# Optimization experiments

Measured on AMD Instinct MI355X. Metric: run time of the kernel, lower is better.

The kernel has to match this reference:

```python
import jax, jax.numpy as jnp
import numpy as np

C = 256          # num_channel
CE = C // 4      # encoded channels = 64
T = 16           # seq_len
K = 7            # filter_size
D = 1            # dilation
G = 4            # num_groups
PAD = ((K - 1) * D) // 2  # 3
K2G = K * K * G  # 196
EPS = 1e-5


def _bn(x, gamma, beta, mean, var):
    # inference-mode BatchNorm3d over channel axis 1
    inv = gamma * jax.lax.rsqrt(var + EPS)
    return x * inv[None, :, None, None, None] + (beta - mean * inv)[None, :, None, None, None]


def _conv1x1(x, w):
    # x: (B, Cin, T, H, W), w: (Cout, Cin) -> (B, Cout, T, H, W)
    return jnp.einsum('bcthw,oc->bothw', x, w)


def _correlation(x, filter_weight):
    # x: (B, CE, T, H, W); filter_weight: (CE, T, K, K)
    B, c, t, h, w = x.shape
    # x1: temporal shift (repeat first frame)
    x1 = jnp.concatenate([x[:, :, :1], x[:, :, :-1]], axis=2)
    x2 = jnp.pad(x, ((0, 0), (0, 0), (0, 0), (PAD, PAD), (PAD, PAD)))
    outs = []
    for ky in range(K):          # dy outer (torch meshgrid 'ij' order)
        for kx in range(K):
            dy, dx = ky * D, kx * D
            wgt = filter_weight[:, :, ky, kx]  # (CE, T)
            r = wgt[None, :, :, None, None] * x1 * x2[:, :, :, dy:dy + h, dx:dx + w]
            r = r.reshape(B, G, c // G, t, h, w).mean(axis=2)  # (B, G, T, H, W)
            outs.append(r)
    return jnp.concatenate(outs, axis=1)  # (B, K^2*G, T, H, W)


def setup_inputs() -> dict:
    key = jax.random.key(0)
    ks = jax.random.split(key, 12)
    B, H, W = 4, 56, 56
    inp = {
        'x': jax.random.normal(ks[0], (B, C, T, H, W), jnp.float32),
        'enc_w': jax.random.normal(ks[1], (CE, C), jnp.float32) * (2.0 / C) ** 0.5,
        'enc_gamma': jax.random.uniform(ks[2], (CE,), jnp.float32, 0.5, 1.5),
        'enc_beta': jax.random.normal(ks[3], (CE,), jnp.float32) * 0.1,
        'enc_mean': jax.random.normal(ks[4], (CE,), jnp.float32) * 0.1,
        'enc_var': jax.random.uniform(ks[5], (CE,), jnp.float32, 0.5, 1.5),
        'filter_weight': jax.random.normal(ks[6], (CE, T, K, K), jnp.float32) * (2.0 / (T * K * K)) ** 0.5,
        'dec_w': jax.random.normal(ks[7], (C, K2G), jnp.float32) * (2.0 / K2G) ** 0.5,
        'dec_gamma': jax.random.uniform(ks[8], (C,), jnp.float32, 0.5, 1.5),
        'dec_beta': jax.random.normal(ks[9], (C,), jnp.float32) * 0.1,
        'dec_mean': jax.random.normal(ks[10], (C,), jnp.float32) * 0.1,
        'dec_var': jax.random.uniform(ks[11], (C,), jnp.float32, 0.5, 1.5),
    }
    return inp


def reference(x, enc_w, enc_gamma, enc_beta, enc_mean, enc_var,
              filter_weight, dec_w, dec_gamma, dec_beta, dec_mean, dec_var):
    x_enc = jax.nn.relu(_bn(_conv1x1(x, enc_w), enc_gamma, enc_beta, enc_mean, enc_var))
    x_corr = _correlation(x_enc, filter_weight)
    x_dec = _bn(_conv1x1(x_corr, dec_w), dec_gamma, dec_beta, dec_mean, dec_var)
    return jax.nn.relu(x + x_dec)
```

## Files before the change

kernel.cpp:

```cpp
#include <hip/hip_runtime.h>

#define CC   256
#define CEE  64
#define TT   16
#define KKK  7
#define PADK 3
#define GGG  4
#define CGP  16
#define K2G  196
#define KPAD 224
#define HHH  56
#define WWW  56
#define HW   3136
#define THW  50176
#define BBB  4

typedef _Float16 f16x8 __attribute__((ext_vector_type(8)));
typedef float    f32x4 __attribute__((ext_vector_type(4)));

#define N_XENC   (BBB*CEE*THW)
#define OFF_XENC 0
#define OFF_EWT  (N_XENC)
#define OFF_ESC  (OFF_EWT + CC*CEE)
#define OFF_ESH  (OFF_ESC + CEE)
#define OFF_DWTH (OFF_ESH + CEE)
#define OFF_DSC  (OFF_DWTH + (CC*KPAD)/2)
#define OFF_DSH  (OFF_DSC + CC)

__global__ void prep_kernel(const float* __restrict__ enc_w,
                            const float* __restrict__ eg, const float* __restrict__ eb,
                            const float* __restrict__ em, const float* __restrict__ ev,
                            const float* __restrict__ dec_w,
                            const float* __restrict__ dg, const float* __restrict__ db,
                            const float* __restrict__ dm, const float* __restrict__ dv,
                            float* __restrict__ ewt, float* __restrict__ esc, float* __restrict__ esh,
                            _Float16* __restrict__ dwth, float* __restrict__ dsc, float* __restrict__ dsh) {
    int i = blockIdx.x * blockDim.x + threadIdx.x;
    int n = blockDim.x * gridDim.x;
    for (int idx = i; idx < CC * CEE; idx += n) {
        int c = idx >> 6, o = idx & 63;
        ewt[idx] = enc_w[o * CC + c];
    }
    for (int idx = i; idx < CC * KPAD; idx += n) {
        int o = idx / KPAD;
        int k = idx - o * KPAD;
        int ky = k >> 5, rem = k & 31, gg = rem >> 3, kx = rem & 7;
        float v = 0.f;
        if (kx < 7) v = dec_w[o * K2G + (ky * 7 + kx) * GGG + gg];
        dwth[idx] = (_Float16)v;
    }
    for (int idx = i; idx < CEE; idx += n) {
        float inv = eg[idx] * rsqrtf(ev[idx] + 1e-5f);
        esc[idx] = inv;
        esh[idx] = eb[idx] - em[idx] * inv;
    }
    for (int idx = i; idx < CC; idx += n) {
        float inv = dg[idx] * rsqrtf(dv[idx] + 1e-5f);
        dsc[idx] = inv;
        dsh[idx] = db[idx] - dm[idx] * inv;
    }
}

__global__ void __launch_bounds__(256) enc_kernel(
        const float* __restrict__ x, const float* __restrict__ ewt,
        const float* __restrict__ esc, const float* __restrict__ esh,
        float* __restrict__ xenc) {
    __shared__ float wlds[64 * 64];
    const int tid  = threadIdx.x;
    const int og   = tid >> 6;
    const int lane = tid & 63;
    const int b    = blockIdx.x / 196;
    const int q0   = (blockIdx.x % 196) * 256 + lane * 4;
    const float* xb = x + (size_t)b * CC * THW + q0;

    f32x4 acc[16];
    #pragma unroll
    for (int i = 0; i < 16; ++i) acc[i] = (f32x4){0.f, 0.f, 0.f, 0.f};

    #pragma unroll 1
    for (int chunk = 0; chunk < 4; ++chunk) {
        __syncthreads();
        const float4* src = (const float4*)(ewt + chunk * 4096);
        float4* dst = (float4*)wlds;
        #pragma unroll
        for (int k = 0; k < 4; ++k) dst[k * 256 + tid] = src[k * 256 + tid];
        __syncthreads();

        f32x4 xv[4];
        #pragma unroll
        for (int u = 0; u < 4; ++u)
            xv[u] = *(const f32x4*)(xb + (size_t)(chunk * 64 + u) * THW);

        #pragma unroll 1
        for (int cb = 0; cb < 16; ++cb) {
            f32x4 xvn[4];
            if (cb < 15) {
                #pragma unroll
                for (int u = 0; u < 4; ++u)
                    xvn[u] = *(const f32x4*)(xb + (size_t)(chunk * 64 + (cb + 1) * 4 + u) * THW);
            }
            #pragma unroll
            for (int u = 0; u < 4; ++u) {
                const f32x4* wr = (const f32x4*)(wlds + (cb * 4 + u) * 64 + og * 16);
                #pragma unroll
                for (int oi4 = 0; oi4 < 4; ++oi4) {
                    f32x4 w4 = wr[oi4];
                    acc[oi4 * 4 + 0] += w4[0] * xv[u];
                    acc[oi4 * 4 + 1] += w4[1] * xv[u];
                    acc[oi4 * 4 + 2] += w4[2] * xv[u];
                    acc[oi4 * 4 + 3] += w4[3] * xv[u];
                }
            }
            if (cb < 15) {
                #pragma unroll
                for (int u = 0; u < 4; ++u) xv[u] = xvn[u];
            }
        }
    }

    const size_t outbase = (size_t)b * CEE * THW + q0;
    #pragma unroll
    for (int oi = 0; oi < 16; ++oi) {
        const int o = og * 16 + oi;
        const float sc = esc[o];
        const float sh = esh[o];
        f32x4 v = acc[oi] * sc + sh;
        #pragma unroll
        for (int r = 0; r < 4; ++r) v[r] = v[r] > 0.f ? v[r] : 0.f;
        *(f32x4*)(xenc + outbase + (size_t)o * THW) = v;
    }
}

__global__ void __launch_bounds__(256, 3) corr_dec_kernel(
        const float* __restrict__ x, const float* __restrict__ xenc,
        const float* __restrict__ fw, const _Float16* __restrict__ dwth,
        const float* __restrict__ dsc, const float* __restrict__ dsh,
        float* __restrict__ out) {
    __shared__ _Float16 x2t[64 * 14 * 16];
    __shared__ float wg[64 * 49];
    __shared__ __align__(16) _Float16 corr_h[64 * 40];

    const int tid = threadIdx.x;
    const int g = tid >> 6;
    const int lane = tid & 63;
    const int ph = lane >> 3;
    const int pw = lane & 7;

    const int bx = blockIdx.x;
    const int tile = bx % 49;
    const int t = (bx / 49) & 15;
    const int b = bx / 784;
    const int th0 = (tile / 7) * 8;
    const int tw0 = (tile % 7) * 8;

    for (int i = tid; i < 64 * 224; i += 256) {
        int c = i / 224;
        int rem = i - c * 224;
        int hy = rem >> 4;
        int hx = rem & 15;
        int h = th0 + hy - PADK;
        int w = tw0 + hx - PADK;
        float v = 0.f;
        if (hx < 14 && (unsigned)h < HHH && (unsigned)w < WWW)
            v = xenc[((b * CEE + c) * TT + t) * HW + h * WWW + w];
        x2t[i] = (_Float16)v;
    }
    for (int i = tid; i < 64 * 49; i += 256) {
        int c = i / 49;
        int o = i - c * 49;
        wg[i] = fw[c * (TT * 49) + t * 49 + o] * (1.f / 16.f);
    }
    const int tprev = t > 0 ? t - 1 : 0;
    const int hwp = (th0 + ph) * WWW + (tw0 + pw);
    float x1r[16];
    #pragma unroll
    for (int j = 0; j < 16; ++j)
        x1r[j] = xenc[((b * CEE + g * CGP + j) * TT + tprev) * HW + hwp];

    f32x4 acc[4][4];
    #pragma unroll
    for (int mi = 0; mi < 4; ++mi)
        #pragma unroll
        for (int ni = 0; ni < 4; ++ni)
            acc[mi][ni] = (f32x4){0.f, 0.f, 0.f, 0.f};

    const int r16 = lane & 15;
    const int quad = lane >> 4;

    __syncthreads();

    #pragma unroll 1
    for (int ky = 0; ky < 7; ++ky) {
        float a[7];
        #pragma unroll
        for (int kx = 0; kx < 7; ++kx) a[kx] = 0.f;
        #pragma unroll
        for (int j = 0; j < 16; ++j) {
            const float x1v = x1r[j];
            const int crow = g * CGP + j;
            const _Float16* x2p = &x2t[(crow * 14 + (ph + ky)) * 16 + pw];
            const float* wrow = &wg[crow * 49 + ky * 7];
            #pragma unroll
            for (int kx = 0; kx < 7; ++kx)
                a[kx] += wrow[kx] * (x1v * (float)x2p[kx]);
        }
        f16x8 pk;
        #pragma unroll
        for (int kx = 0; kx < 7; ++kx) pk[kx] = (_Float16)a[kx];
        pk[7] = (_Float16)0.f;
        *(f16x8*)(corr_h + lane * 40 + g * 8) = pk;

        f16x8 af[4];
        #pragma unroll
        for (int mi = 0; mi < 4; ++mi)
            af[mi] = *(const f16x8*)(dwth + (size_t)(g * 64 + mi * 16 + r16) * KPAD
                                     + ky * 32 + quad * 8);

        __syncthreads();

        f16x8 bf[4];
        #pragma unroll
        for (int ni = 0; ni < 4; ++ni)
            bf[ni] = *(const f16x8*)(corr_h + (ni * 16 + r16) * 40 + quad * 8);
        #pragma unroll
        for (int mi = 0; mi < 4; ++mi)
            #pragma unroll
            for (int ni = 0; ni < 4; ++ni)
                acc[mi][ni] = __builtin_amdgcn_mfma_f32_16x16x32_f16(af[mi], bf[ni],
                                                                     acc[mi][ni], 0, 0, 0);
        __syncthreads();
    }

    #pragma unroll
    for (int mi = 0; mi < 4; ++mi) {
        #pragma unroll
        for (int reg = 0; reg < 4; ++reg) {
            const int o = g * 64 + mi * 16 + quad * 4 + reg;
            const float sc = dsc[o];
            const float sh = dsh[o];
            const int obase = ((b * CC + o) * TT + t) * HW;
            #pragma unroll
            for (int ni = 0; ni < 4; ++ni) {
                const int p = ni * 16 + r16;
                const int idx = obase + (th0 + (p >> 3)) * WWW + tw0 + (p & 7);
                float v = acc[mi][ni][reg] * sc + sh;
                float rr = x[idx] + v;
                out[idx] = rr > 0.f ? rr : 0.f;
            }
        }
    }
}

extern "C" void kernel_launch(void* const* d_in, const int* in_sizes, int n_in,
                              void* d_out, int out_size, void* d_ws, size_t ws_size,
                              hipStream_t stream) {
    const float* x     = (const float*)d_in[0];
    const float* enc_w = (const float*)d_in[1];
    const float* eg    = (const float*)d_in[2];
    const float* eb    = (const float*)d_in[3];
    const float* em    = (const float*)d_in[4];
    const float* ev    = (const float*)d_in[5];
    const float* fw    = (const float*)d_in[6];
    const float* dec_w = (const float*)d_in[7];
    const float* dg    = (const float*)d_in[8];
    const float* db    = (const float*)d_in[9];
    const float* dm    = (const float*)d_in[10];
    const float* dv    = (const float*)d_in[11];
    float* out = (float*)d_out;
    float* ws  = (float*)d_ws;

    prep_kernel<<<104, 256, 0, stream>>>(enc_w, eg, eb, em, ev, dec_w, dg, db, dm, dv,
                                         ws + OFF_EWT, ws + OFF_ESC, ws + OFF_ESH,
                                         (_Float16*)(ws + OFF_DWTH),
                                         ws + OFF_DSC, ws + OFF_DSH);
    enc_kernel<<<784, 256, 0, stream>>>(x, ws + OFF_EWT, ws + OFF_ESC, ws + OFF_ESH,
                                        ws + OFF_XENC);
    corr_dec_kernel<<<3136, 256, 0, stream>>>(x, ws + OFF_XENC, fw,
                                              (const _Float16*)(ws + OFF_DWTH),
                                              ws + OFF_DSC, ws + OFF_DSH,
                                              out);
}
```

Before: 849.3 us.

## Run encoder 1x1 conv on FP16 MFMA and batch corr-kernel staging loads

The encoder conv is rewritten to use 16x16x32 f16 MFMA with fp16 weights laid out in a padded buffer. x is converted to fp16 in registers instead of running the fp32 FMA loop with LDS-staged weights, and the grid doubles to 1568 blocks. In the corr/dec kernel the xenc and filter-weight staging loads are batched into registers before the LDS stores, and the dwth fragment loads move earlier to hide latency. Its launch-bounds occupancy hint is also removed. Reduced input precision in the encoder may add numeric error.

```diff
diff --git a/kernel.cpp b/kernel.cpp
--- a/kernel.cpp
+++ b/kernel.cpp
@@ -9,6 +9,7 @@
 #define CGP  16
 #define K2G  196
 #define KPAD 224
+#define EWP  264
 #define HHH  56
 #define WWW  56
 #define HW   3136
@@ -20,12 +21,12 @@
 
 #define N_XENC   (BBB*CEE*THW)
 #define OFF_XENC 0
-#define OFF_EWT  (N_XENC)
-#define OFF_ESC  (OFF_EWT + CC*CEE)
+#define OFF_ESC  (N_XENC)
 #define OFF_ESH  (OFF_ESC + CEE)
 #define OFF_DWTH (OFF_ESH + CEE)
 #define OFF_DSC  (OFF_DWTH + (CC*KPAD)/2)
 #define OFF_DSH  (OFF_DSC + CC)
+#define OFF_EWH  (OFF_DSH + CC)
 
 __global__ void prep_kernel(const float* __restrict__ enc_w,
                             const float* __restrict__ eg, const float* __restrict__ eb,
@@ -33,13 +34,14 @@
                             const float* __restrict__ dec_w,
                             const float* __restrict__ dg, const float* __restrict__ db,
                             const float* __restrict__ dm, const float* __restrict__ dv,
-                            float* __restrict__ ewt, float* __restrict__ esc, float* __restrict__ esh,
+                            _Float16* __restrict__ ewh, float* __restrict__ esc, float* __restrict__ esh,
                             _Float16* __restrict__ dwth, float* __restrict__ dsc, float* __restrict__ dsh) {
     int i = blockIdx.x * blockDim.x + threadIdx.x;
     int n = blockDim.x * gridDim.x;
-    for (int idx = i; idx < CC * CEE; idx += n) {
-        int c = idx >> 6, o = idx & 63;
-        ewt[idx] = enc_w[o * CC + c];
+    for (int idx = i; idx < CEE * EWP; idx += n) {
+        int o = idx / EWP;
+        int k = idx - o * EWP;
+        ewh[idx] = (k < CC) ? (_Float16)enc_w[o * CC + k] : (_Float16)0.f;
     }
     for (int idx = i; idx < CC * KPAD; idx += n) {
         int o = idx / KPAD;
@@ -61,77 +63,71 @@
     }
 }
 
-__global__ void __launch_bounds__(256) enc_kernel(
-        const float* __restrict__ x, const float* __restrict__ ewt,
+__global__ void __launch_bounds__(256, 3) enc_kernel(
+        const float* __restrict__ x, const _Float16* __restrict__ ewh,
         const float* __restrict__ esc, const float* __restrict__ esh,
         float* __restrict__ xenc) {
-    __shared__ float wlds[64 * 64];
     const int tid  = threadIdx.x;
-    const int og   = tid >> 6;
+    const int w    = tid >> 6;
     const int lane = tid & 63;
-    const int b    = blockIdx.x / 196;
-    const int q0   = (blockIdx.x % 196) * 256 + lane * 4;
-    const float* xb = x + (size_t)b * CC * THW + q0;
-
-    f32x4 acc[16];
-    #pragma unroll
-    for (int i = 0; i < 16; ++i) acc[i] = (f32x4){0.f, 0.f, 0.f, 0.f};
-
-    #pragma unroll 1
-    for (int chunk = 0; chunk < 4; ++chunk) {
-        __syncthreads();
-        const float4* src = (const float4*)(ewt + chunk * 4096);
-        float4* dst = (float4*)wlds;
-        #pragma unroll
-        for (int k = 0; k < 4; ++k) dst[k * 256 + tid] = src[k * 256 + tid];
-        __syncthreads();
-
-        f32x4 xv[4];
-        #pragma unroll
-        for (int u = 0; u < 4; ++u)
-            xv[u] = *(const f32x4*)(xb + (size_t)(chunk * 64 + u) * THW);
-
-        #pragma unroll 1
-        for (int cb = 0; cb < 16; ++cb) {
-            f32x4 xvn[4];
-            if (cb < 15) {
-                #pragma unroll
-                for (int u = 0; u < 4; ++u)
-                    xvn[u] = *(const f32x4*)(xb + (size_t)(chunk * 64 + (cb + 1) * 4 + u) * THW);
+    const int r16  = lane & 15;
+    const int quad = lane >> 4;
+    const int b    = blockIdx.x / 392;
+    const int q0   = (blockIdx.x % 392) * 128 + w * 32;
+    const float* xb = x + (size_t)b * CC * THW;
+
+    f32x4 acc[4][2];
+    #pragma unroll
+    for (int mi = 0; mi < 4; ++mi)
+        #pragma unroll
+        for (int ni = 0; ni < 2; ++ni)
+            acc[mi][ni] = (f32x4){0.f, 0.f, 0.f, 0.f};
+
+    #pragma unroll
+    for (int kc = 0; kc < 8; ++kc) {
+        f16x8 af[4];
+        #pragma unroll
+        for (int mi = 0; mi < 4; ++mi)
+            af[mi] = *(const f16x8*)(ewh + (mi * 16 + r16) * EWP + kc * 32 + quad * 8);
+
+        f16x8 bf[2];
+        #pragma unroll
+        for (int ni = 0; ni < 2; ++ni) {
+            float xv[8];
+            #pragma unroll
+            for (int j = 0; j < 8; ++j)
+                xv[j] = xb[(size_t)(kc * 32 + quad * 8 + j) * THW + q0 + ni * 16 + r16];
+            #pragma unroll
+            for (int j = 0; j < 8; ++j)
+                bf[ni][j] = (_Float16)xv[j];
+        }
+
+        #pragma unroll
+        for (int mi = 0; mi < 4; ++mi)
+            #pragma unroll
+            for (int ni = 0; ni < 2; ++ni)
+                acc[mi][ni] = __builtin_amdgcn_mfma_f32_16x16x32_f16(af[mi], bf[ni],
+                                                                     acc[mi][ni], 0, 0, 0);
+    }
+
+    #pragma unroll
+    for (int mi = 0; mi < 4; ++mi) {
+        #pragma unroll
+        for (int reg = 0; reg < 4; ++reg) {
+            const int o = mi * 16 + quad * 4 + reg;
+            const float sc = esc[o];
+            const float sh = esh[o];
+            #pragma unroll
+            for (int ni = 0; ni < 2; ++ni) {
+                const int q = q0 + ni * 16 + r16;
+                float v = acc[mi][ni][reg] * sc + sh;
+                xenc[(size_t)(b * CEE + o) * THW + q] = v > 0.f ? v : 0.f;
             }
-            #pragma unroll
-            for (int u = 0; u < 4; ++u) {
-                const f32x4* wr = (const f32x4*)(wlds + (cb * 4 + u) * 64 + og * 16);
-                #pragma unroll
-                for (int oi4 = 0; oi4 < 4; ++oi4) {
-                    f32x4 w4 = wr[oi4];
-                    acc[oi4 * 4 + 0] += w4[0] * xv[u];
-                    acc[oi4 * 4 + 1] += w4[1] * xv[u];
-                    acc[oi4 * 4 + 2] += w4[2] * xv[u];
-                    acc[oi4 * 4 + 3] += w4[3] * xv[u];
-                }
-            }
-            if (cb < 15) {
-                #pragma unroll
-                for (int u = 0; u < 4; ++u) xv[u] = xvn[u];
-            }
-        }
-    }
-
-    const size_t outbase = (size_t)b * CEE * THW + q0;
-    #pragma unroll
-    for (int oi = 0; oi < 16; ++oi) {
-        const int o = og * 16 + oi;
-        const float sc = esc[o];
-        const float sh = esh[o];
-        f32x4 v = acc[oi] * sc + sh;
-        #pragma unroll
-        for (int r = 0; r < 4; ++r) v[r] = v[r] > 0.f ? v[r] : 0.f;
-        *(f32x4*)(xenc + outbase + (size_t)o * THW) = v;
+        }
     }
 }
 
-__global__ void __launch_bounds__(256, 3) corr_dec_kernel(
+__global__ void __launch_bounds__(256) corr_dec_kernel(
         const float* __restrict__ x, const float* __restrict__ xenc,
         const float* __restrict__ fw, const _Float16* __restrict__ dwth,
         const float* __restrict__ dsc, const float* __restrict__ dsh,
@@ -153,22 +149,46 @@
     const int th0 = (tile / 7) * 8;
     const int tw0 = (tile % 7) * 8;
 
-    for (int i = tid; i < 64 * 224; i += 256) {
-        int c = i / 224;
-        int rem = i - c * 224;
-        int hy = rem >> 4;
-        int hx = rem & 15;
-        int h = th0 + hy - PADK;
-        int w = tw0 + hx - PADK;
-        float v = 0.f;
-        if (hx < 14 && (unsigned)h < HHH && (unsigned)w < WWW)
-            v = xenc[((b * CEE + c) * TT + t) * HW + h * WWW + w];
-        x2t[i] = (_Float16)v;
-    }
-    for (int i = tid; i < 64 * 49; i += 256) {
-        int c = i / 49;
-        int o = i - c * 49;
-        wg[i] = fw[c * (TT * 49) + t * 49 + o] * (1.f / 16.f);
+    {
+        const int bbase = (b * CEE * TT + t) * HW;
+        #pragma unroll 1
+        for (int k0 = 0; k0 < 56; k0 += 8) {
+            float v[8];
+            #pragma unroll
+            for (int u = 0; u < 8; ++u) {
+                int i = tid + (k0 + u) * 256;
+                int c = i / 224;
+                int rem = i - c * 224;
+                int hy = rem >> 4;
+                int hx = rem & 15;
+                int h = th0 + hy - PADK;
+                int w = tw0 + hx - PADK;
+                bool ok = (hx < 14) && ((unsigned)h < HHH) && ((unsigned)w < WWW);
+                v[u] = ok ? xenc[bbase + c * (TT * HW) + h * WWW + w] : 0.f;
+            }
+            #pragma unroll
+            for (int u = 0; u < 8; ++u)
+                x2t[tid + (k0 + u) * 256] = (_Float16)v[u];
+        }
+    }
+    {
+        float v[12];
+        #pragma unroll
+        for (int u = 0; u < 12; ++u) {
+            int i = tid + u * 256;
+            int c = i / 49;
+            int o = i - c * 49;
+            v[u] = fw[c * (TT * 49) + t * 49 + o] * (1.f / 16.f);
+        }
+        #pragma unroll
+        for (int u = 0; u < 12; ++u)
+            wg[tid + u * 256] = v[u];
+        if (tid < 64) {
+            int i = tid + 3072;
+            int c = i / 49;
+            int o = i - c * 49;
+            wg[i] = fw[c * (TT * 49) + t * 49 + o] * (1.f / 16.f);
+        }
     }
     const int tprev = t > 0 ? t - 1 : 0;
     const int hwp = (th0 + ph) * WWW + (tw0 + pw);
@@ -191,6 +211,12 @@
 
     #pragma unroll 1
     for (int ky = 0; ky < 7; ++ky) {
+        f16x8 af[4];
+        #pragma unroll
+        for (int mi = 0; mi < 4; ++mi)
+            af[mi] = *(const f16x8*)(dwth + (size_t)(g * 64 + mi * 16 + r16) * KPAD
+                                     + ky * 32 + quad * 8);
+
         float a[7];
         #pragma unroll
         for (int kx = 0; kx < 7; ++kx) a[kx] = 0.f;
@@ -209,12 +235,6 @@
         for (int kx = 0; kx < 7; ++kx) pk[kx] = (_Float16)a[kx];
         pk[7] = (_Float16)0.f;
         *(f16x8*)(corr_h + lane * 40 + g * 8) = pk;
-
-        f16x8 af[4];
-        #pragma unroll
-        for (int mi = 0; mi < 4; ++mi)
-            af[mi] = *(const f16x8*)(dwth + (size_t)(g * 64 + mi * 16 + r16) * KPAD
-                                     + ky * 32 + quad * 8);
 
         __syncthreads();
 
@@ -270,11 +290,13 @@
     float* ws  = (float*)d_ws;
 
     prep_kernel<<<104, 256, 0, stream>>>(enc_w, eg, eb, em, ev, dec_w, dg, db, dm, dv,
-                                         ws + OFF_EWT, ws + OFF_ESC, ws + OFF_ESH,
+                                         (_Float16*)(ws + OFF_EWH),
+                                         ws + OFF_ESC, ws + OFF_ESH,
                                          (_Float16*)(ws + OFF_DWTH),
                                          ws + OFF_DSC, ws + OFF_DSH);
-    enc_kernel<<<784, 256, 0, stream>>>(x, ws + OFF_EWT, ws + OFF_ESC, ws + OFF_ESH,
-                                        ws + OFF_XENC);
+    enc_kernel<<<1568, 256, 0, stream>>>(x, (const _Float16*)(ws + OFF_EWH),
+                                         ws + OFF_ESC, ws + OFF_ESH,
+                                         ws + OFF_XENC);
     corr_dec_kernel<<<3136, 256, 0, stream>>>(x, ws + OFF_XENC, fw,
                                               (const _Float16*)(ws + OFF_DWTH),
                                               ws + OFF_DSC, ws + OFF_DSH,
```

Result: faster. 831.5 us (-2.1%).
